# Kernel tuning notes

Hardware: AMD Instinct MI355X
Metric: run time of the kernel (lower is better)

## Reference

```python
import jax, jax.numpy as jnp
import numpy as np
from jax import lax

MAX_NUM_LEVELS = 3.5
MIN_LEVEL = 0.0
# torch computes num_levels = ceil(levels.max())+1 (data-dependent); since levels are
# clamped to max_num_levels-1 = 2.5, the static upper bound is ceil(2.5)+1 = 4.
# Building the full stack is mathematically identical (gather selects the same levels).
NUM_LEVELS = int(np.ceil(MAX_NUM_LEVELS - 1.0)) + 1  # = 4


def _blur_filter():
    f = np.array([1.0, 3.0, 3.0, 1.0])
    k = f[:, None] * f[None, :]
    k = k / k.sum()
    return jnp.asarray(k, jnp.float32)  # [4,4]


def _downsample_2x(x):
    # reflect-pad 1, depthwise 4x4 Gaussian conv, stride 2  -> [N,C,H/2,W/2]
    N, C, H, W = x.shape
    k = jnp.tile(_blur_filter()[None, None], (C, 1, 1, 1))  # [C,1,4,4]
    xp = jnp.pad(x, ((0, 0), (0, 0), (1, 1), (1, 1)), mode='reflect')
    return lax.conv_general_dilated(xp, k.astype(x.dtype), (2, 2), 'VALID',
                                    feature_group_count=C)


def _upsample(x, scale):
    # bilinear, align_corners=False (half-pixel centers) == jax.image.resize 'bilinear'
    N, C, H, W = x.shape
    return jax.image.resize(x, (N, C, int(H * scale), int(W * scale)), method='bilinear')


def _max_coord_distance(coords):
    # coords [N,H,W,2] -> max neighbor distance [N,H,W] (replication-padded neighbors)
    cp = jnp.pad(coords, ((0, 0), (1, 1), (1, 1), (0, 0)), mode='edge')
    cl = cp[:, 1:-1, :-2]
    cr = cp[:, 1:-1, 2:]
    cu = cp[:, :-2, 1:-1]
    cd = cp[:, 2:, 1:-1]

    def _dist(o):
        sq = jnp.sum((o - coords) ** 2, axis=-1)
        return jnp.sqrt(jnp.clip(sq, 1.0, None))

    return jnp.maximum(jnp.maximum(_dist(cl), _dist(cr)),
                       jnp.maximum(_dist(cu), _dist(cd)))


def _grid_sample_border(img, grid):
    # img [N,K,H,W], grid [N,Ho,Wo,2] in [-1,1]; bilinear, align_corners=False,
    # padding_mode='border' (coords clamped to valid range before interpolation)
    N, K, H, W = img.shape
    ix = jnp.clip(((grid[..., 0] + 1.0) * W - 1.0) / 2.0, 0.0, W - 1.0)
    iy = jnp.clip(((grid[..., 1] + 1.0) * H - 1.0) / 2.0, 0.0, H - 1.0)
    x0f, y0f = jnp.floor(ix), jnp.floor(iy)
    wx = (ix - x0f)[:, None]  # [N,1,Ho,Wo]
    wy = (iy - y0f)[:, None]
    x0 = x0f.astype(jnp.int32)
    y0 = y0f.astype(jnp.int32)
    x1 = jnp.clip(x0 + 1, 0, W - 1)
    y1 = jnp.clip(y0 + 1, 0, H - 1)

    def _gather(im, yi, xi):  # im [K,H,W] -> [K,Ho,Wo]
        return im[:, yi, xi]

    g = jax.vmap(_gather)
    v00 = g(img, y0, x0)
    v01 = g(img, y0, x1)
    v10 = g(img, y1, x0)
    v11 = g(img, y1, x1)
    return (v00 * (1 - wx) + v01 * wx) * (1 - wy) + (v10 * (1 - wx) + v11 * wx) * wy


def setup_inputs() -> dict:
    key = jax.random.key(0)
    k1, k2 = jax.random.split(key)
    N, C, H, W = 4, 96, 256, 256
    inputs = jax.random.normal(k1, (N, C, H, W), dtype=jnp.float32)
    # identity grid + mild random warp -> realistic spread of LOD levels
    ys = (jnp.arange(H, dtype=jnp.float32) + 0.5) / H * 2.0 - 1.0
    xs = (jnp.arange(W, dtype=jnp.float32) + 0.5) / W * 2.0 - 1.0
    gy, gx = jnp.meshgrid(ys, xs, indexing='ij')
    ident = jnp.stack([gx, gy], axis=-1)[None]  # [1,H,W,2]
    noise = (jax.random.uniform(k2, (N, H, W, 2), dtype=jnp.float32) * 2.0 - 1.0) * 0.05
    grid = jnp.clip(ident + noise, -1.0, 1.0)
    return {"inputs": inputs, "grid": grid}


def reference(inputs, grid):
    N, C, H, W = inputs.shape
    Ho, Wo = grid.shape[1], grid.shape[2]
    # absolute-pixel coords of the sampling grid
    xc = (W - 1.0) * (grid[..., 0] + 1.0) / 2.0
    yc = (H - 1.0) * (grid[..., 1] + 1.0) / 2.0
    coords = jnp.stack([xc, yc], axis=-1)  # [N,Ho,Wo,2]
    levels = jnp.clip(jnp.log2(_max_coord_distance(coords)), 0.0, MAX_NUM_LEVELS - 1.0)
    levels = jnp.clip(levels, MIN_LEVEL, None)  # [N,Ho,Wo]

    # Gaussian stack: blur+downsample, then bilinear-upsample back to full res
    lvl_imgs = [inputs]
    cur = inputs
    for i in range(1, NUM_LEVELS):
        cur = _downsample_2x(cur)
        lvl_imgs.append(_upsample(cur, 2.0 ** i))
    stack = jnp.stack(lvl_imgs, axis=2)  # [N,C,D,H,W]
    D = stack.shape[2]

    # warp all levels at once
    warped = _grid_sample_border(stack.reshape(N, C * D, H, W), grid)
    warped = warped.reshape(N, C, D, Ho, Wo)

    # per-pixel trilinear LOD blend
    l0 = jnp.floor(levels).astype(jnp.int32)
    l1 = jnp.ceil(levels).astype(jnp.int32)
    idx0 = jnp.broadcast_to(l0[:, None, None], (N, C, 1, Ho, Wo))
    idx1 = jnp.broadcast_to(l1[:, None, None], (N, C, 1, Ho, Wo))
    o0 = jnp.take_along_axis(warped, idx0, axis=2)[:, :, 0]
    o1 = jnp.take_along_axis(warped, idx1, axis=2)[:, :, 0]
    w = (levels - jnp.floor(levels))[:, None]  # [N,1,Ho,Wo], == levels % 1.0
    return o0 + w * (o1 - o0)
```

## Files before the change

### kernel.cpp

```cpp
#include <hip/hip_runtime.h>
#include <math.h>

namespace {

constexpr int N = 4, C = 96, H = 256, W = 256;
constexpr int HW = H * W;
constexpr float LMAX = 2.5f;

typedef float v4 __attribute__((ext_vector_type(4)));
struct __attribute__((packed, aligned(4))) V4U { v4 v; };
__device__ inline v4 load4u(const float* p) {
  return reinterpret_cast<const V4U*>(p)->v;
}
__device__ inline int refl(int i, int S) {
  i = i < 0 ? -i : i;
  return i >= S ? 2 * S - 2 - i : i;
}

__global__ __launch_bounds__(256) void downsample1(
    const float* __restrict__ in, float* __restrict__ out) {
  __shared__ float s[68 * 68];
  const int Wi = 256, Wo = 128, T = 4;
  int tile = blockIdx.x, nc = blockIdx.y;
  int tx0 = (tile % T) * 32, ty0 = (tile / T) * 32;
  int ix0 = 2 * tx0 - 2, iy0 = 2 * ty0 - 2;
  const float* p = in + (size_t)nc * Wi * Wi;
  int tid = threadIdx.x;

  for (int k = 0; k < 5; k++) {
    int ch = tid + 256 * k;
    if (ch < 68 * 17) {
      int yy = ch / 17, cx = (ch - 17 * yy) * 4;
      int gy = refl(iy0 + yy, Wi);
      int gx = ix0 + cx;
      const float* rowp = p + (size_t)gy * Wi;
      float* sp = s + yy * 68 + cx;
      if (gx >= 0 && gx + 3 < Wi) {
        v4 t = load4u(rowp + gx);
        sp[0] = t.x; sp[1] = t.y; sp[2] = t.z; sp[3] = t.w;
      } else {
#pragma unroll
        for (int j = 0; j < 4; j++) sp[j] = rowp[refl(gx + j, Wi)];
      }
    }
  }
  __syncthreads();

  const float fw[4] = {0.125f, 0.375f, 0.375f, 0.125f};
  int dx = tid & 31, dy0 = tid >> 5;
  float* po = out + (size_t)nc * Wo * Wo;
#pragma unroll
  for (int r = 0; r < 4; r++) {
    int dy = dy0 + 8 * r;
    float acc = 0.0f;
#pragma unroll
    for (int a = 0; a < 4; a++) {
      const float* row = s + (2 * dy + 1 + a) * 68 + 2 * dx + 1;
      acc = fmaf(fw[a],
                 fmaf(fw[0], row[0],
                 fmaf(fw[1], row[1],
                 fmaf(fw[2], row[2], fw[3] * row[3]))), acc);
    }
    po[(size_t)(ty0 + dy) * Wo + tx0 + dx] = acc;
  }
}

__global__ __launch_bounds__(256) void downsample23(
    const float* __restrict__ pyr1, float* __restrict__ pyr2,
    float* __restrict__ pyr3) {
  __shared__ float s1[70 * 72];
  __shared__ float h2[70 * 36];
  __shared__ float p2[34 * 36];
  __shared__ float h3[34 * 16];
  int t = blockIdx.x, nc = blockIdx.y;
  int t3x = (t & 1) * 16, t3y = (t >> 1) * 16;
  int u0x = 2 * t3x - 1, u0y = 2 * t3y - 1;
  int v0x = 2 * u0x - 1, v0y = 2 * u0y - 1;
  const float* p1 = pyr1 + (size_t)nc * 128 * 128;
  int tid = threadIdx.x;
  const float fw[4] = {0.125f, 0.375f, 0.375f, 0.125f};

  for (int k = 0; k < 20; k++) {
    int e = tid + 256 * k;
    if (e < 4900) {
      int yy = e / 70, xx = e - 70 * yy;
      s1[yy * 72 + xx] =
          p1[(size_t)refl(v0y + yy, 128) * 128 + refl(v0x + xx, 128)];
    }
  }
  __syncthreads();

  for (int k = 0; k < 10; k++) {
    int e = tid + 256 * k;
    if (e < 70 * 34) {
      int r = e / 34, c = e - 34 * r;
      const float* sp = s1 + r * 72 + 2 * c;
      h2[r * 36 + c] = fmaf(fw[0], sp[0],
                       fmaf(fw[1], sp[1],
                       fmaf(fw[2], sp[2], fw[3] * sp[3])));
    }
  }
  __syncthreads();

  for (int k = 0; k < 5; k++) {
    int e = tid + 256 * k;
    if (e < 34 * 34) {
      int r = e / 34, c = e - 34 * r;
      const float* hp = h2 + (2 * r) * 36 + c;
      p2[r * 36 + c] = fmaf(fw[0], hp[0],
                       fmaf(fw[1], hp[36],
                       fmaf(fw[2], hp[72], fw[3] * hp[108])));
    }
  }
  __syncthreads();

  float* o2 = pyr2 + (size_t)nc * 64 * 64;
#pragma unroll
  for (int k = 0; k < 4; k++) {
    int e = tid + 256 * k;
    int yy = e >> 5, xx = e & 31;
    o2[(size_t)(2 * t3y + yy) * 64 + 2 * t3x + xx] = p2[(yy + 1) * 36 + xx + 1];
  }

  for (int k = 0; k < 3; k++) {
    int e = tid + 256 * k;
    if (e < 34 * 16) {
      int r = e >> 4, c = e & 15;
      float acc = 0.f;
#pragma unroll
      for (int kk = 0; kk < 4; kk++) {
        int j = refl(2 * (t3x + c) - 1 + kk, 64) - u0x;
        acc = fmaf(fw[kk], p2[r * 36 + j], acc);
      }
      h3[r * 16 + c] = acc;
    }
  }
  __syncthreads();

  {
    int yy = tid >> 4, xx = tid & 15;
    float acc = 0.f;
#pragma unroll
    for (int kk = 0; kk < 4; kk++) {
      int j = refl(2 * (t3y + yy) - 1 + kk, 64) - u0y;
      acc = fmaf(fw[kk], h3[j * 16 + xx], acc);
    }
    pyr3[(size_t)nc * 32 * 32 + (t3y + yy) * 32 + t3x + xx] = acc;
  }
}

__device__ inline void axis3(int q0, int q1, float wq, int l, int S,
                             int* ii, float* ww) {
  float inv = 1.0f / (float)(1 << l);
  float pos0 = ((float)q0 + 0.5f) * inv - 0.5f;
  float pos1 = ((float)q1 + 0.5f) * inv - 0.5f;
  int p0 = (int)floorf(pos0), p1 = (int)floorf(pos1);
  float f0 = pos0 - (float)p0, f1 = pos1 - (float)p1;
  int a0 = min(max(p0, 0), S - 1), a1 = min(max(p0 + 1, 0), S - 1);
  int b0 = min(max(p1, 0), S - 1), b1 = min(max(p1 + 1, 0), S - 1);
  int base = min(a0, b0);
  float w0 = 0.f, w1 = 0.f, w2 = 0.f;
  float v; int s;
  v = (1.0f - wq) * (1.0f - f0); s = a0 - base;
  w0 += (s == 0) ? v : 0.f; w1 += (s == 1) ? v : 0.f; w2 += (s == 2) ? v : 0.f;
  v = (1.0f - wq) * f0;          s = a1 - base;
  w0 += (s == 0) ? v : 0.f; w1 += (s == 1) ? v : 0.f; w2 += (s == 2) ? v : 0.f;
  v = wq * (1.0f - f1);          s = b0 - base;
  w0 += (s == 0) ? v : 0.f; w1 += (s == 1) ? v : 0.f; w2 += (s == 2) ? v : 0.f;
  v = wq * f1;                   s = b1 - base;
  w0 += (s == 0) ? v : 0.f; w1 += (s == 1) ? v : 0.f; w2 += (s == 2) ? v : 0.f;
  ii[0] = base;
  ii[1] = min(base + 1, S - 1);
  ii[2] = min(base + 2, S - 1);
  ww[0] = w0; ww[1] = w1; ww[2] = w2;
}

constexpr int L2OFF = 8192, L3OFF = 11392, LDSTOT = 12544;

__global__ __launch_bounds__(256, 3) void gather_tiled(
    const float* __restrict__ inputs, const float* __restrict__ grid,
    const float* __restrict__ pyr1, const float* __restrict__ pyr2,
    const float* __restrict__ pyr3, float* __restrict__ out) {
  __shared__ __align__(16) float lds[LDSTOT];
  int tile = blockIdx.x, g = blockIdx.y, n = blockIdx.z;
  int tx0 = (tile & 15) << 4, ty0 = (tile >> 4) << 4;
  int gb = g * 32;
  int tid = threadIdx.x;

  int px = tid & 15, py = tid >> 4;
  int x = tx0 + px, y = ty0 + py;

  const float2* gp = reinterpret_cast<const float2*>(grid) + (size_t)n * HW;
  float2 gc = gp[y * W + x];
  float2 gl = gp[y * W + max(x - 1, 0)];
  float2 gr = gp[y * W + min(x + 1, W - 1)];
  float2 gu = gp[max(y - 1, 0) * W + x];
  float2 gd = gp[min(y + 1, H - 1) * W + x];

  int rsx1 = min(max((tx0 >> 1) - 4, 0), 128 - 16);
  int rsy1 = min(max((ty0 >> 1) - 4, 0), 128 - 16);
  int rsx2 = min(max((tx0 >> 2) - 3, 0), 64 - 10);
  int rsy2 = min(max((ty0 >> 2) - 3, 0), 64 - 10);
  int rsx3 = min(max((tx0 >> 3) - 2, 0), 32 - 6);
  int rsy3 = min(max((ty0 >> 3) - 2, 0), 32 - 6);

  {
    const float* base = pyr1 + ((size_t)(n * C + gb)) * (128 * 128);
#pragma unroll
    for (int k = 0; k < 32; k++) {
      int e = tid + 256 * k;
      int c = e >> 8, tf = e & 255;
      int yy = tf >> 4, xx = tf & 15;
      float t = base[(size_t)c * (128 * 128) + (rsy1 + yy) * 128 + rsx1 + xx];
      lds[(c >> 2) * 1024 + tf * 4 + (c & 3)] = t;
    }
  }
  {
    const float* base = pyr2 + ((size_t)(n * C + gb)) * (64 * 64);
    for (int k = 0; k < 13; k++) {
      int e = tid + 256 * k;
      if (e < 3200) {
        int c = e / 100, tf = e - 100 * c;
        int yy = tf / 10, xx = tf - 10 * yy;
        float t = base[(size_t)c * (64 * 64) + (rsy2 + yy) * 64 + rsx2 + xx];
        lds[L2OFF + (c >> 2) * 400 + tf * 4 + (c & 3)] = t;
      }
    }
  }
  {
    const float* base = pyr3 + ((size_t)(n * C + gb)) * (32 * 32);
    for (int k = 0; k < 5; k++) {
      int e = tid + 256 * k;
      if (e < 1152) {
        int c = e / 36, tf = e - 36 * c;
        int yy = tf / 6, xx = tf - 6 * yy;
        float t = base[(size_t)c * (32 * 32) + (rsy3 + yy) * 32 + rsx3 + xx];
        lds[L3OFF + (c >> 2) * 144 + tf * 4 + (c & 3)] = t;
      }
    }
  }
  __syncthreads();

  float lv;
  {
    float cx = 255.0f * (gc.x + 1.0f) * 0.5f;
    float cy = 255.0f * (gc.y + 1.0f) * 0.5f;
    float m = 1.0f;
    float2 nb[4] = {gl, gr, gu, gd};
#pragma unroll
    for (int i = 0; i < 4; i++) {
      float ox = 255.0f * (nb[i].x + 1.0f) * 0.5f - cx;
      float oy = 255.0f * (nb[i].y + 1.0f) * 0.5f - cy;
      m = fmaxf(m, ox * ox + oy * oy);
    }
    lv = fminf(fmaxf(0.5f * __log2f(m), 0.0f), LMAX);
  }

  float ix = fminf(fmaxf(fmaf(gc.x + 1.0f, 128.0f, -0.5f), 0.0f), 255.0f);
  float iy = fminf(fmaxf(fmaf(gc.y + 1.0f, 128.0f, -0.5f), 0.0f), 255.0f);
  int x0 = (int)floorf(ix); float wx = ix - (float)x0; int x1 = min(x0 + 1, 255);
  int y0 = (int)floorf(iy); float wy = iy - (float)y0; int y1 = min(y0 + 1, 255);

  float lf = floorf(lv);
  int l0 = (int)lf;
  float wl = lv - lf;
  float wlA = 1.0f - wl;
  int lB = l0 + 1;

  auto meta = [&](int l, int& off, int& sz, int& rw, int& rx, int& ry, int& S) {
    if (l == 1)      { off = 0;     sz = 256; rw = 16; rx = rsx1; ry = rsy1; S = 128; }
    else if (l == 2) { off = L2OFF; sz = 100; rw = 10; rx = rsx2; ry = rsy2; S = 64; }
    else             { off = L3OFF; sz = 36;  rw = 6;  rx = rsx3; ry = rsy3; S = 32; }
  };

  int offB, szB, rwB, rxB, ryB, SB;
  meta(lB, offB, szB, rwB, rxB, ryB, SB);
  int tfB[9]; float wB[9];
  {
    int xi[3]; float xw[3]; axis3(x0, x1, wx, lB, SB, xi, xw);
    int yi[3]; float yw[3]; axis3(y0, y1, wy, lB, SB, yi, yw);
#pragma unroll
    for (int r = 0; r < 3; r++)
#pragma unroll
      for (int cc = 0; cc < 3; cc++) {
        int ry_ = min(max(yi[r] - ryB, 0), rwB - 1);
        int rx_ = min(max(xi[cc] - rxB, 0), rwB - 1);
        tfB[r * 3 + cc] = ry_ * rwB + rx_;
        wB[r * 3 + cc] = yw[r] * xw[cc] * wl;
      }
  }

  float* po = out + ((size_t)(n * C + gb)) * HW + (size_t)y * W + x;

  if (l0 >= 1) {
    int offA, szA, rwA, rxA, ryA, SA;
    meta(l0, offA, szA, rwA, rxA, ryA, SA);
    int tfA[9]; float wA[9];
    {
      int xi[3]; float xw[3]; axis3(x0, x1, wx, l0, SA, xi, xw);
      int yi[3]; float yw[3]; axis3(y0, y1, wy, l0, SA, yi, yw);
#pragma unroll
      for (int r = 0; r < 3; r++)
#pragma unroll
        for (int cc = 0; cc < 3; cc++) {
          int ry_ = min(max(yi[r] - ryA, 0), rwA - 1);
          int rx_ = min(max(xi[cc] - rxA, 0), rwA - 1);
          tfA[r * 3 + cc] = ry_ * rwA + rx_;
          wA[r * 3 + cc] = yw[r] * xw[cc] * wlA;
        }
    }
#pragma unroll
    for (int q = 0; q < 8; q++) {
      const float* pA = lds + offA + q * szA * 4;
      const float* pB = lds + offB + q * szB * 4;
      v4 acc = {0.f, 0.f, 0.f, 0.f};
#pragma unroll
      for (int t = 0; t < 9; t++)
        acc += *reinterpret_cast<const v4*>(pA + tfA[t] * 4) * wA[t];
#pragma unroll
      for (int t = 0; t < 9; t++)
        acc += *reinterpret_cast<const v4*>(pB + tfB[t] * 4) * wB[t];
      float* pq = po + (size_t)(4 * q) * HW;
      pq[0] = acc.x; pq[HW] = acc.y;
      pq[2 * (size_t)HW] = acc.z; pq[3 * (size_t)HW] = acc.w;
    }
  } else {
    const float* inA = inputs + ((size_t)(n * C + gb)) * HW;
#pragma unroll 1
    for (int q = 0; q < 8; q++) {
      const float* pB = lds + offB + q * szB * 4;
      v4 accB = {0.f, 0.f, 0.f, 0.f};
#pragma unroll
      for (int t = 0; t < 9; t++)
        accB += *reinterpret_cast<const v4*>(pB + tfB[t] * 4) * wB[t];
      float av[4];
#pragma unroll
      for (int j = 0; j < 4; j++) {
        const float* ip = inA + (size_t)(4 * q + j) * HW;
        float v00 = ip[y0 * W + x0], v01 = ip[y0 * W + x1];
        float v10 = ip[y1 * W + x0], v11 = ip[y1 * W + x1];
        av[j] = (v00 * (1.f - wx) + v01 * wx) * (1.f - wy) +
                (v10 * (1.f - wx) + v11 * wx) * wy;
      }
      v4 o = {fmaf(av[0], wlA, accB.x), fmaf(av[1], wlA, accB.y),
              fmaf(av[2], wlA, accB.z), fmaf(av[3], wlA, accB.w)};
      float* pq = po + (size_t)(4 * q) * HW;
      pq[0] = o.x; pq[HW] = o.y;
      pq[2 * (size_t)HW] = o.z; pq[3 * (size_t)HW] = o.w;
    }
  }
}

}

extern "C" void kernel_launch(void* const* d_in, const int* in_sizes, int n_in,
                              void* d_out, int out_size, void* d_ws, size_t ws_size,
                              hipStream_t stream) {
  const float* inputs = (const float*)d_in[0];
  const float* grid = (const float*)d_in[1];
  float* out = (float*)d_out;
  float* ws = (float*)d_ws;

  float* pyr1 = ws;
  float* pyr2 = pyr1 + (size_t)N * C * 128 * 128;
  float* pyr3 = pyr2 + (size_t)N * C * 64 * 64;

  int NC = N * C;
  downsample1<<<dim3(16, NC), 256, 0, stream>>>(inputs, pyr1);
  downsample23<<<dim3(4, NC), 256, 0, stream>>>(pyr1, pyr2, pyr3);
  gather_tiled<<<dim3(256, 3, N), 256, 0, stream>>>(inputs, grid,
                                                    pyr1, pyr2, pyr3, out);
}
```

Before: 256.2 us.

## Drop pyr1 LDS staging and gather level-1 directly from global memory

The gather kernel no longer stages the level-1 pyramid tile (32 channels of 16x16) into LDS. Level-1 samples are now read directly from global memory via the 9-tap footprint, with separate code paths for level pairs (0,1), (1,2) and (2,3). This cuts LDS use to about 17 KB, which allows launch bounds of 6 blocks per CU instead of 3, and it removes the bulk pyr1 load that many pixels never use. The cost is uncached, scattered global reads for level-1 pixels and more divergent per-channel loops.

```diff
diff --git a/kernel.cpp b/kernel.cpp
--- a/kernel.cpp
+++ b/kernel.cpp
@@ -175,9 +175,9 @@
   ww[0] = w0; ww[1] = w1; ww[2] = w2;
 }
 
-constexpr int L2OFF = 8192, L3OFF = 11392, LDSTOT = 12544;
-
-__global__ __launch_bounds__(256, 3) void gather_tiled(
+constexpr int L3OFF = 3200, LDSTOT = 4352;
+
+__global__ __launch_bounds__(256, 6) void gather_tiled(
     const float* __restrict__ inputs, const float* __restrict__ grid,
     const float* __restrict__ pyr1, const float* __restrict__ pyr2,
     const float* __restrict__ pyr3, float* __restrict__ out) {
@@ -197,24 +197,11 @@
   float2 gu = gp[max(y - 1, 0) * W + x];
   float2 gd = gp[min(y + 1, H - 1) * W + x];
 
-  int rsx1 = min(max((tx0 >> 1) - 4, 0), 128 - 16);
-  int rsy1 = min(max((ty0 >> 1) - 4, 0), 128 - 16);
   int rsx2 = min(max((tx0 >> 2) - 3, 0), 64 - 10);
   int rsy2 = min(max((ty0 >> 2) - 3, 0), 64 - 10);
   int rsx3 = min(max((tx0 >> 3) - 2, 0), 32 - 6);
   int rsy3 = min(max((ty0 >> 3) - 2, 0), 32 - 6);
 
-  {
-    const float* base = pyr1 + ((size_t)(n * C + gb)) * (128 * 128);
-#pragma unroll
-    for (int k = 0; k < 32; k++) {
-      int e = tid + 256 * k;
-      int c = e >> 8, tf = e & 255;
-      int yy = tf >> 4, xx = tf & 15;
-      float t = base[(size_t)c * (128 * 128) + (rsy1 + yy) * 128 + rsx1 + xx];
-      lds[(c >> 2) * 1024 + tf * 4 + (c & 3)] = t;
-    }
-  }
   {
     const float* base = pyr2 + ((size_t)(n * C + gb)) * (64 * 64);
     for (int k = 0; k < 13; k++) {
@@ -223,7 +210,7 @@
         int c = e / 100, tf = e - 100 * c;
         int yy = tf / 10, xx = tf - 10 * yy;
         float t = base[(size_t)c * (64 * 64) + (rsy2 + yy) * 64 + rsx2 + xx];
-        lds[L2OFF + (c >> 2) * 400 + tf * 4 + (c & 3)] = t;
+        lds[(c >> 2) * 400 + tf * 4 + (c & 3)] = t;
       }
     }
   }
@@ -267,52 +254,28 @@
   float wlA = 1.0f - wl;
   int lB = l0 + 1;
 
-  auto meta = [&](int l, int& off, int& sz, int& rw, int& rx, int& ry, int& S) {
-    if (l == 1)      { off = 0;     sz = 256; rw = 16; rx = rsx1; ry = rsy1; S = 128; }
-    else if (l == 2) { off = L2OFF; sz = 100; rw = 10; rx = rsx2; ry = rsy2; S = 64; }
-    else             { off = L3OFF; sz = 36;  rw = 6;  rx = rsx3; ry = rsy3; S = 32; }
-  };
-
-  int offB, szB, rwB, rxB, ryB, SB;
-  meta(lB, offB, szB, rwB, rxB, ryB, SB);
-  int tfB[9]; float wB[9];
-  {
-    int xi[3]; float xw[3]; axis3(x0, x1, wx, lB, SB, xi, xw);
-    int yi[3]; float yw[3]; axis3(y0, y1, wy, lB, SB, yi, yw);
+  float* po = out + ((size_t)(n * C + gb)) * HW + (size_t)y * W + x;
+
+  if (l0 == 2) {
+    int xiA[3]; float xwA[3]; axis3(x0, x1, wx, 2, 64, xiA, xwA);
+    int yiA[3]; float ywA[3]; axis3(y0, y1, wy, 2, 64, yiA, ywA);
+    int xiB[3]; float xwB[3]; axis3(x0, x1, wx, 3, 32, xiB, xwB);
+    int yiB[3]; float ywB[3]; axis3(y0, y1, wy, 3, 32, yiB, ywB);
+    int tfA[9]; float wA[9];
+    int tfB[9]; float wB[9];
 #pragma unroll
     for (int r = 0; r < 3; r++)
 #pragma unroll
       for (int cc = 0; cc < 3; cc++) {
-        int ry_ = min(max(yi[r] - ryB, 0), rwB - 1);
-        int rx_ = min(max(xi[cc] - rxB, 0), rwB - 1);
-        tfB[r * 3 + cc] = ry_ * rwB + rx_;
-        wB[r * 3 + cc] = yw[r] * xw[cc] * wl;
-      }
-  }
-
-  float* po = out + ((size_t)(n * C + gb)) * HW + (size_t)y * W + x;
-
-  if (l0 >= 1) {
-    int offA, szA, rwA, rxA, ryA, SA;
-    meta(l0, offA, szA, rwA, rxA, ryA, SA);
-    int tfA[9]; float wA[9];
-    {
-      int xi[3]; float xw[3]; axis3(x0, x1, wx, l0, SA, xi, xw);
-      int yi[3]; float yw[3]; axis3(y0, y1, wy, l0, SA, yi, yw);
-#pragma unroll
-      for (int r = 0; r < 3; r++)
-#pragma unroll
-        for (int cc = 0; cc < 3; cc++) {
-          int ry_ = min(max(yi[r] - ryA, 0), rwA - 1);
-          int rx_ = min(max(xi[cc] - rxA, 0), rwA - 1);
-          tfA[r * 3 + cc] = ry_ * rwA + rx_;
-          wA[r * 3 + cc] = yw[r] * xw[cc] * wlA;
-        }
-    }
+        tfA[r * 3 + cc] = (yiA[r] - rsy2) * 10 + (xiA[cc] - rsx2);
+        wA[r * 3 + cc] = ywA[r] * xwA[cc] * wlA;
+        tfB[r * 3 + cc] = (yiB[r] - rsy3) * 6 + (xiB[cc] - rsx3);
+        wB[r * 3 + cc] = ywB[r] * xwB[cc] * wl;
+      }
 #pragma unroll
     for (int q = 0; q < 8; q++) {
-      const float* pA = lds + offA + q * szA * 4;
-      const float* pB = lds + offB + q * szB * 4;
+      const float* pA = lds + q * 400;
+      const float* pB = lds + L3OFF + q * 144;
       v4 acc = {0.f, 0.f, 0.f, 0.f};
 #pragma unroll
       for (int t = 0; t < 9; t++)
@@ -325,28 +288,69 @@
       pq[2 * (size_t)HW] = acc.z; pq[3 * (size_t)HW] = acc.w;
     }
   } else {
+    int goA[9]; float wAg[9];
+    if (l0 == 1) {
+      int xi[3]; float xw[3]; axis3(x0, x1, wx, 1, 128, xi, xw);
+      int yi[3]; float yw[3]; axis3(y0, y1, wy, 1, 128, yi, yw);
+#pragma unroll
+      for (int r = 0; r < 3; r++)
+#pragma unroll
+        for (int cc = 0; cc < 3; cc++) {
+          goA[r * 3 + cc] = yi[r] * 128 + xi[cc];
+          wAg[r * 3 + cc] = yw[r] * xw[cc];
+        }
+    }
+    int tfB[9]; float wB[9];
+    int goB[9];
+    if (lB == 2) {
+      int xi[3]; float xw[3]; axis3(x0, x1, wx, 2, 64, xi, xw);
+      int yi[3]; float yw[3]; axis3(y0, y1, wy, 2, 64, yi, yw);
+#pragma unroll
+      for (int r = 0; r < 3; r++)
+#pragma unroll
+        for (int cc = 0; cc < 3; cc++) {
+          tfB[r * 3 + cc] = (yi[r] - rsy2) * 10 + (xi[cc] - rsx2);
+          wB[r * 3 + cc] = yw[r] * xw[cc];
+        }
+    } else {
+      int xi[3]; float xw[3]; axis3(x0, x1, wx, 1, 128, xi, xw);
+      int yi[3]; float yw[3]; axis3(y0, y1, wy, 1, 128, yi, yw);
+#pragma unroll
+      for (int r = 0; r < 3; r++)
+#pragma unroll
+        for (int cc = 0; cc < 3; cc++) {
+          goB[r * 3 + cc] = yi[r] * 128 + xi[cc];
+          wB[r * 3 + cc] = yw[r] * xw[cc];
+        }
+    }
+    const float* p1n = pyr1 + ((size_t)(n * C + gb)) * (128 * 128);
     const float* inA = inputs + ((size_t)(n * C + gb)) * HW;
 #pragma unroll 1
-    for (int q = 0; q < 8; q++) {
-      const float* pB = lds + offB + q * szB * 4;
-      v4 accB = {0.f, 0.f, 0.f, 0.f};
-#pragma unroll
-      for (int t = 0; t < 9; t++)
-        accB += *reinterpret_cast<const v4*>(pB + tfB[t] * 4) * wB[t];
-      float av[4];
-#pragma unroll
-      for (int j = 0; j < 4; j++) {
-        const float* ip = inA + (size_t)(4 * q + j) * HW;
+    for (int c = 0; c < 32; c++) {
+      float a;
+      if (l0 == 1) {
+        const float* pc = p1n + (size_t)c * (128 * 128);
+        a = 0.f;
+#pragma unroll
+        for (int t = 0; t < 9; t++) a = fmaf(wAg[t], pc[goA[t]], a);
+      } else {
+        const float* ip = inA + (size_t)c * HW;
         float v00 = ip[y0 * W + x0], v01 = ip[y0 * W + x1];
         float v10 = ip[y1 * W + x0], v11 = ip[y1 * W + x1];
-        av[j] = (v00 * (1.f - wx) + v01 * wx) * (1.f - wy) +
-                (v10 * (1.f - wx) + v11 * wx) * wy;
-      }
-      v4 o = {fmaf(av[0], wlA, accB.x), fmaf(av[1], wlA, accB.y),
-              fmaf(av[2], wlA, accB.z), fmaf(av[3], wlA, accB.w)};
-      float* pq = po + (size_t)(4 * q) * HW;
-      pq[0] = o.x; pq[HW] = o.y;
-      pq[2 * (size_t)HW] = o.z; pq[3 * (size_t)HW] = o.w;
+        a = (v00 * (1.f - wx) + v01 * wx) * (1.f - wy) +
+            (v10 * (1.f - wx) + v11 * wx) * wy;
+      }
+      float b = 0.f;
+      if (lB == 2) {
+        const float* pB = lds + (c >> 2) * 400 + (c & 3);
+#pragma unroll
+        for (int t = 0; t < 9; t++) b = fmaf(wB[t], pB[tfB[t] * 4], b);
+      } else {
+        const float* pc = p1n + (size_t)c * (128 * 128);
+#pragma unroll
+        for (int t = 0; t < 9; t++) b = fmaf(wB[t], pc[goB[t]], b);
+      }
+      po[(size_t)c * HW] = fmaf(wl, b - a, a);
     }
   }
 }
```

New measurement: 437.7 us. +70.9%, slower.
